# Optimization experiments

Measured on AMD Instinct MI355X. Metric: run time of the kernel, lower is better.

Reference implementation:

```python
import jax, jax.numpy as jnp
import numpy as np

N_NODES = 100000
N_EDGES = 1600000
N_GRAPHS = 256


def gcn_conv(x, src, dst, edge_weight, W, b, num_nodes):
    """PyG GCNConv: add self-loops, symmetric degree normalization,
    linear transform, scatter-add aggregation, bias."""
    loop = jnp.arange(num_nodes)
    s = jnp.concatenate([src, loop])
    d = jnp.concatenate([dst, loop])
    ew = jnp.concatenate([edge_weight, jnp.ones((num_nodes,), dtype=edge_weight.dtype)])
    deg = jax.ops.segment_sum(ew, d, num_segments=num_nodes)  # [N]
    dinv = jnp.where(deg > 0, deg ** -0.5, 0.0)
    norm = dinv[s] * ew * dinv[d]  # [E+N]
    h = x @ W  # [N, out]
    msg = h[s] * norm[:, None]  # gather + scale
    out = jax.ops.segment_sum(msg, d, num_segments=num_nodes)  # scatter-add
    return out + b


def global_mean_pool(x, batch, num_graphs):
    s = jax.ops.segment_sum(x, batch, num_segments=num_graphs)
    cnt = jax.ops.segment_sum(jnp.ones((x.shape[0],), dtype=x.dtype), batch, num_segments=num_graphs)
    return s / jnp.maximum(cnt, 1.0)[:, None]


def setup_inputs() -> dict:
    key = jax.random.key(0)
    ks = jax.random.split(key, 12)
    x = jax.random.normal(ks[0], (N_NODES, 128), dtype=jnp.float32)
    edge_index = jax.random.randint(ks[1], (2, N_EDGES), 0, N_NODES, dtype=jnp.int64)
    edge_attr = jax.random.uniform(ks[2], (N_EDGES,), dtype=jnp.float32)
    batch = jnp.sort(jax.random.randint(ks[3], (N_NODES,), 0, N_GRAPHS, dtype=jnp.int64))
    def lin(k, fan_in, fan_out):
        lim = 1.0 / np.sqrt(fan_in)
        kw, kb = jax.random.split(k)
        W = jax.random.uniform(kw, (fan_in, fan_out), minval=-lim, maxval=lim, dtype=jnp.float32)
        b = jax.random.uniform(kb, (fan_out,), minval=-lim, maxval=lim, dtype=jnp.float32)
        return W, b
    W1, b1 = lin(ks[4], 128, 64)
    W2, b2 = lin(ks[5], 64, 64)
    W3, b3 = lin(ks[6], 64, 64)
    Wl, bl = lin(ks[7], 64, 10)
    return {"x": x, "edge_index": edge_index, "edge_attr": edge_attr, "batch": batch,
            "W1": W1, "b1": b1, "W2": W2, "b2": b2, "W3": W3, "b3": b3, "Wl": Wl, "bl": bl}


def reference(x, edge_index, edge_attr, batch, W1, b1, W2, b2, W3, b3, Wl, bl):
    src, dst = edge_index[0], edge_index[1]
    n = x.shape[0]
    h = jax.nn.relu(gcn_conv(x, src, dst, edge_attr, W1, b1, n))
    h = jax.nn.relu(gcn_conv(h, src, dst, edge_attr, W2, b2, n))
    h = jax.nn.relu(gcn_conv(h, src, dst, edge_attr, W3, b3, n))
    g = global_mean_pool(h, batch, N_GRAPHS)  # [G, 64]
    return g @ Wl + bl  # [G, num_classes]
```

## Files before the change

### kernel.cpp

```cpp
#include <hip/hip_runtime.h>
#include <hip/hip_bf16.h>

#define N_NODES  100000
#define N_EDGES  1600000
#define N_GRAPHS 256
#define F 64
#define NBUCK  782
#define CHUNK  4096
#define NCHUNK 391


__global__ __launch_bounds__(1024) void k_hist(const int* __restrict__ dst, int* __restrict__ hist) {
    __shared__ int lh[NBUCK];
    int tid = threadIdx.x, chunk = blockIdx.x;
    for (int j = tid; j < NBUCK; j += 1024) lh[j] = 0;
    __syncthreads();
    int e0 = chunk * CHUNK;
#pragma unroll
    for (int i = 0; i < CHUNK / 1024; i++) {
        int e = e0 + i * 1024 + tid;
        if (e < N_EDGES) atomicAdd(&lh[dst[e] >> 7], 1);
    }
    __syncthreads();
    for (int j = tid; j < NBUCK; j += 1024) hist[chunk * NBUCK + j] = lh[j];
}

__global__ __launch_bounds__(512) void k_colscan(int* __restrict__ hist, int* __restrict__ btot) {
    __shared__ int ts[512];
    int b = blockIdx.x, tid = threadIdx.x;
    int v = (tid < NCHUNK) ? hist[tid * NBUCK + b] : 0;
    ts[tid] = v;
    __syncthreads();
    int x = v;
    for (int off = 1; off < 512; off <<= 1) {
        int t = (tid >= off) ? ts[tid - off] : 0;
        __syncthreads();
        x += t; ts[tid] = x;
        __syncthreads();
    }
    if (tid < NCHUNK) hist[tid * NBUCK + b] = x - v;
    if (tid == 511) btot[b] = x;
}

__global__ __launch_bounds__(256) void k_bscan(const int* __restrict__ btot, int* __restrict__ base) {
    __shared__ int ts[256];
    int tid = threadIdx.x;
    int v[4], loc[4], run = 0;
#pragma unroll
    for (int k = 0; k < 4; k++) {
        int c = tid * 4 + k;
        v[k] = (c < NBUCK) ? btot[c] : 0;
        loc[k] = run; run += v[k];
    }
    ts[tid] = run;
    __syncthreads();
    int x = run;
    for (int off = 1; off < 256; off <<= 1) {
        int t = (tid >= off) ? ts[tid - off] : 0;
        __syncthreads();
        x += t; ts[tid] = x;
        __syncthreads();
    }
    int texcl = x - run;
#pragma unroll
    for (int k = 0; k < 4; k++) {
        int c = tid * 4 + k;
        if (c < NBUCK) base[c] = texcl + loc[k];
    }
    if (tid == 255) base[NBUCK] = x;
}

__global__ __launch_bounds__(1024) void k_partition(const int* __restrict__ src, const int* __restrict__ dst,
                                                    const float* __restrict__ ew,
                                                    const int* __restrict__ hist, const int* __restrict__ base,
                                                    long long* __restrict__ part) {
    __shared__ int cursor[NBUCK];
    int tid = threadIdx.x, chunk = blockIdx.x;
    for (int j = tid; j < NBUCK; j += 1024) cursor[j] = base[j] + hist[chunk * NBUCK + j];
    __syncthreads();
    int e0 = chunk * CHUNK;
#pragma unroll
    for (int i = 0; i < CHUNK / 1024; i++) {
        int e = e0 + i * 1024 + tid;
        if (e < N_EDGES) {
            int d = dst[e];
            int pos = atomicAdd(&cursor[d >> 7], 1);
            unsigned lo = (unsigned)src[e] | ((unsigned)(d & 127) << 17);
            long long rec = (long long)((unsigned long long)lo |
                            ((unsigned long long)__float_as_uint(ew[e]) << 32));
            part[pos] = rec;
        }
    }
}

__global__ __launch_bounds__(256) void k_bucket(const long long* __restrict__ part,
                                                const int* __restrict__ base,
                                                float* __restrict__ dinv_g, int* __restrict__ row_off,
                                                int2* __restrict__ esec) {
    __shared__ float fdeg[128];
    __shared__ float sdinv[128];
    __shared__ int   cnt[128];
    __shared__ int   sc[128];
    __shared__ int   cursor[128];
    int b = blockIdx.x, tid = threadIdx.x;
    if (tid < 128) { fdeg[tid] = 1.0f; cnt[tid] = 0; }
    __syncthreads();
    int e0 = base[b], e1 = base[b + 1], ne = e1 - e0;
    for (int k = tid; k < ne; k += 256) {
        long long rec = part[e0 + k];
        int lo = (int)rec;
        int d7 = (lo >> 17) & 127;
        atomicAdd(&fdeg[d7], __uint_as_float((unsigned)(rec >> 32)));
        atomicAdd(&cnt[d7], 1);
    }
    __syncthreads();
    int myc = 0, x = 0;
    if (tid < 128) {
        float dv = rsqrtf(fdeg[tid]);
        sdinv[tid] = dv;
        int node = b * 128 + tid;
        if (node < N_NODES) dinv_g[node] = dv;
        myc = cnt[tid]; x = myc; sc[tid] = x;
    }
    __syncthreads();
    for (int off = 1; off < 128; off <<= 1) {
        int t = (tid < 128 && tid >= off) ? sc[tid - off] : 0;
        __syncthreads();
        if (tid < 128) { x += t; sc[tid] = x; }
        __syncthreads();
    }
    if (tid < 128) {
        int excl = x - myc;
        int node = b * 128 + tid;
        if (node < N_NODES) row_off[node] = e0 + excl;
        cursor[tid] = e0 + excl;
    }
    if (b == 0 && tid == 0) row_off[N_NODES] = N_EDGES;
    __syncthreads();
    for (int k = tid; k < ne; k += 256) {
        long long rec = part[e0 + k];
        int lo = (int)rec;
        int d7 = (lo >> 17) & 127;
        float w = __uint_as_float((unsigned)(rec >> 32));
        int pos = atomicAdd(&cursor[d7], 1);
        esec[pos] = make_int2((lo & 0x1FFFF) << 7, __float_as_int(w * sdinv[d7]));
    }
}

__global__ void k_coef(int2* __restrict__ esec, const float* __restrict__ dinv_g) {
    int e = blockIdx.x * 256 + threadIdx.x;
    if (e < N_EDGES) {
        int2 v = esec[e];
        esec[e] = make_int2(v.x, __float_as_int(__int_as_float(v.y) * dinv_g[((unsigned)v.x) >> 7]));
    } else if (e < N_EDGES + 16) {
        esec[e] = make_int2(0, 0);
    }
}

__global__ void k_gstart(const int* __restrict__ batch, int* gstart) {
    int g = blockIdx.x * 256 + threadIdx.x;
    if (g > N_GRAPHS) return;
    int lo = 0, hi = N_NODES;
    while (lo < hi) {
        int mid = (lo + hi) >> 1;
        if (batch[mid] < g) lo = mid + 1; else hi = mid;
    }
    gstart[g] = lo;
}

template <int K, bool BF16IN>
__global__ __launch_bounds__(256) void k_gemm(const void* __restrict__ Xv,
                                              const float* __restrict__ W,
                                              __hip_bfloat16* __restrict__ H) {
    constexpr int KC = 32;
    constexpr int XP = KC + 4;
    __shared__ float Xs[128 * XP];
    __shared__ float Ws[KC * F];
    const int tid  = threadIdx.x;
    const int fgrp = tid & 15;
    const int ngrp = tid >> 4;
    const int f0   = fgrp * 4;
    const int nb   = blockIdx.x * 128;

    float acc[8][4];
#pragma unroll
    for (int i = 0; i < 8; i++)
#pragma unroll
        for (int j = 0; j < 4; j++) acc[i][j] = 0.0f;

    for (int kc = 0; kc < K; kc += KC) {
        if (kc) __syncthreads();
        if (BF16IN) {
            const unsigned short* X = (const unsigned short*)Xv;
#pragma unroll
            for (int pass = 0; pass < 2; pass++) {
                int idx = tid + pass * 256;
                int r = idx >> 2, q = idx & 3;
                int gr = nb + r; if (gr >= N_NODES) gr = N_NODES - 1;
                uint4 v = *(const uint4*)&X[(size_t)gr * K + kc + q * 8];
                float* dp = &Xs[r * XP + q * 8];
                dp[0] = __uint_as_float(v.x << 16);
                dp[1] = __uint_as_float(v.x & 0xffff0000u);
                dp[2] = __uint_as_float(v.y << 16);
                dp[3] = __uint_as_float(v.y & 0xffff0000u);
                dp[4] = __uint_as_float(v.z << 16);
                dp[5] = __uint_as_float(v.z & 0xffff0000u);
                dp[6] = __uint_as_float(v.w << 16);
                dp[7] = __uint_as_float(v.w & 0xffff0000u);
            }
        } else {
            const float* X = (const float*)Xv;
#pragma unroll
            for (int pass = 0; pass < 4; pass++) {
                int idx = tid + pass * 256;
                int r = idx >> 3, q = idx & 7;
                int gr = nb + r; if (gr >= N_NODES) gr = N_NODES - 1;
                float4 v = *(const float4*)&X[(size_t)gr * K + kc + q * 4];
                *(float4*)&Xs[r * XP + q * 4] = v;
            }
        }
#pragma unroll
        for (int pass = 0; pass < 2; pass++) {
            int idx = tid + pass * 256;
            float4 v = *(const float4*)&W[(size_t)(kc + (idx >> 4)) * F + (idx & 15) * 4];
            *(float4*)&Ws[idx * 4] = v;
        }
        __syncthreads();
#pragma unroll
        for (int k = 0; k < KC; k += 4) {
            float4 wv[4];
#pragma unroll
            for (int kk = 0; kk < 4; kk++)
                wv[kk] = *(const float4*)&Ws[(k + kk) * F + f0];
#pragma unroll
            for (int i = 0; i < 8; i++) {
                float4 xv = *(const float4*)&Xs[(ngrp + 16 * i) * XP + k];
                acc[i][0] = fmaf(xv.x, wv[0].x, acc[i][0]);
                acc[i][0] = fmaf(xv.y, wv[1].x, acc[i][0]);
                acc[i][0] = fmaf(xv.z, wv[2].x, acc[i][0]);
                acc[i][0] = fmaf(xv.w, wv[3].x, acc[i][0]);
                acc[i][1] = fmaf(xv.x, wv[0].y, acc[i][1]);
                acc[i][1] = fmaf(xv.y, wv[1].y, acc[i][1]);
                acc[i][1] = fmaf(xv.z, wv[2].y, acc[i][1]);
                acc[i][1] = fmaf(xv.w, wv[3].y, acc[i][1]);
                acc[i][2] = fmaf(xv.x, wv[0].z, acc[i][2]);
                acc[i][2] = fmaf(xv.y, wv[1].z, acc[i][2]);
                acc[i][2] = fmaf(xv.z, wv[2].z, acc[i][2]);
                acc[i][2] = fmaf(xv.w, wv[3].z, acc[i][2]);
                acc[i][3] = fmaf(xv.x, wv[0].w, acc[i][3]);
                acc[i][3] = fmaf(xv.y, wv[1].w, acc[i][3]);
                acc[i][3] = fmaf(xv.z, wv[2].w, acc[i][3]);
                acc[i][3] = fmaf(xv.w, wv[3].w, acc[i][3]);
            }
        }
    }
#pragma unroll
    for (int i = 0; i < 8; i++) {
        int gn = nb + ngrp + 16 * i;
        if (gn < N_NODES) {
            __hip_bfloat16 hb[4];
            hb[0] = __float2bfloat16(acc[i][0]);
            hb[1] = __float2bfloat16(acc[i][1]);
            hb[2] = __float2bfloat16(acc[i][2]);
            hb[3] = __float2bfloat16(acc[i][3]);
            *(uint2*)&H[(size_t)gn * F + f0] = *(uint2*)hb;
        }
    }
}

__global__ __launch_bounds__(256) void k_agg(const __hip_bfloat16* __restrict__ H,
                                             const int* __restrict__ row_off,
                                             const int2* __restrict__ esec,
                                             const float* __restrict__ dinv,
                                             const float* __restrict__ bias,
                                             __hip_bfloat16* __restrict__ O) {
    int wv   = threadIdx.x >> 6;
    int lane = threadIdx.x & 63;
    int np   = blockIdx.x * 16 + wv * 4;
    int q  = lane >> 3;
    int f8 = lane & 7;
    int r0 = __builtin_amdgcn_readfirstlane(row_off[np]);
    int r1 = __builtin_amdgcn_readfirstlane(row_off[np + 1]);
    int r2 = __builtin_amdgcn_readfirstlane(row_off[np + 2]);
    int r3 = __builtin_amdgcn_readfirstlane(row_off[np + 3]);
    int r4 = __builtin_amdgcn_readfirstlane(row_off[np + 4]);
    const char* Hbase = (const char*)H;

    float a0[8], a1[8], a2[8], a3[8];
#pragma unroll
    for (int u = 0; u < 8; u++) { a0[u] = 0.0f; a1[u] = 0.0f; a2[u] = 0.0f; a3[u] = 0.0f; }

    int l0 = r1 - r0, l1 = r2 - r1, l2 = r3 - r2, l3 = r4 - r3;
    int ml = l0 > l1 ? l0 : l1;
    if (l2 > ml) ml = l2;
    if (l3 > ml) ml = l3;
    int iters = (ml + 7) >> 3;
    int j0 = r0 + q, j1 = r1 + q, j2 = r2 + q, j3 = r3 + q;
    for (int it = 0; it < iters; it++, j0 += 8, j1 += 8, j2 += 8, j3 += 8) {
        int i0 = j0 < N_EDGES ? j0 : N_EDGES;
        int i1 = j1 < N_EDGES ? j1 : N_EDGES;
        int i2 = j2 < N_EDGES ? j2 : N_EDGES;
        int i3 = j3 < N_EDGES ? j3 : N_EDGES;
        int2 ev0 = esec[i0];
        int2 ev1 = esec[i1];
        int2 ev2 = esec[i2];
        int2 ev3 = esec[i3];
        float c0 = (j0 < r1) ? __int_as_float(ev0.y) : 0.0f;
        float c1 = (j1 < r2) ? __int_as_float(ev1.y) : 0.0f;
        float c2 = (j2 < r3) ? __int_as_float(ev2.y) : 0.0f;
        float c3 = (j3 < r4) ? __int_as_float(ev3.y) : 0.0f;
        uint4 h0 = *(const uint4*)(Hbase + (unsigned)ev0.x + (f8 << 4));
        uint4 h1 = *(const uint4*)(Hbase + (unsigned)ev1.x + (f8 << 4));
        uint4 h2 = *(const uint4*)(Hbase + (unsigned)ev2.x + (f8 << 4));
        uint4 h3 = *(const uint4*)(Hbase + (unsigned)ev3.x + (f8 << 4));
        a0[0] = fmaf(c0, __uint_as_float(h0.x << 16),         a0[0]);
        a0[1] = fmaf(c0, __uint_as_float(h0.x & 0xffff0000u), a0[1]);
        a0[2] = fmaf(c0, __uint_as_float(h0.y << 16),         a0[2]);
        a0[3] = fmaf(c0, __uint_as_float(h0.y & 0xffff0000u), a0[3]);
        a0[4] = fmaf(c0, __uint_as_float(h0.z << 16),         a0[4]);
        a0[5] = fmaf(c0, __uint_as_float(h0.z & 0xffff0000u), a0[5]);
        a0[6] = fmaf(c0, __uint_as_float(h0.w << 16),         a0[6]);
        a0[7] = fmaf(c0, __uint_as_float(h0.w & 0xffff0000u), a0[7]);
        a1[0] = fmaf(c1, __uint_as_float(h1.x << 16),         a1[0]);
        a1[1] = fmaf(c1, __uint_as_float(h1.x & 0xffff0000u), a1[1]);
        a1[2] = fmaf(c1, __uint_as_float(h1.y << 16),         a1[2]);
        a1[3] = fmaf(c1, __uint_as_float(h1.y & 0xffff0000u), a1[3]);
        a1[4] = fmaf(c1, __uint_as_float(h1.z << 16),         a1[4]);
        a1[5] = fmaf(c1, __uint_as_float(h1.z & 0xffff0000u), a1[5]);
        a1[6] = fmaf(c1, __uint_as_float(h1.w << 16),         a1[6]);
        a1[7] = fmaf(c1, __uint_as_float(h1.w & 0xffff0000u), a1[7]);
        a2[0] = fmaf(c2, __uint_as_float(h2.x << 16),         a2[0]);
        a2[1] = fmaf(c2, __uint_as_float(h2.x & 0xffff0000u), a2[1]);
        a2[2] = fmaf(c2, __uint_as_float(h2.y << 16),         a2[2]);
        a2[3] = fmaf(c2, __uint_as_float(h2.y & 0xffff0000u), a2[3]);
        a2[4] = fmaf(c2, __uint_as_float(h2.z << 16),         a2[4]);
        a2[5] = fmaf(c2, __uint_as_float(h2.z & 0xffff0000u), a2[5]);
        a2[6] = fmaf(c2, __uint_as_float(h2.w << 16),         a2[6]);
        a2[7] = fmaf(c2, __uint_as_float(h2.w & 0xffff0000u), a2[7]);
        a3[0] = fmaf(c3, __uint_as_float(h3.x << 16),         a3[0]);
        a3[1] = fmaf(c3, __uint_as_float(h3.x & 0xffff0000u), a3[1]);
        a3[2] = fmaf(c3, __uint_as_float(h3.y << 16),         a3[2]);
        a3[3] = fmaf(c3, __uint_as_float(h3.y & 0xffff0000u), a3[3]);
        a3[4] = fmaf(c3, __uint_as_float(h3.z << 16),         a3[4]);
        a3[5] = fmaf(c3, __uint_as_float(h3.z & 0xffff0000u), a3[5]);
        a3[6] = fmaf(c3, __uint_as_float(h3.w << 16),         a3[6]);
        a3[7] = fmaf(c3, __uint_as_float(h3.w & 0xffff0000u), a3[7]);
    }
#pragma unroll
    for (int m = 8; m < 64; m <<= 1) {
#pragma unroll
        for (int u = 0; u < 8; u++) {
            a0[u] += __shfl_xor(a0[u], m);
            a1[u] += __shfl_xor(a1[u], m);
            a2[u] += __shfl_xor(a2[u], m);
            a3[u] += __shfl_xor(a3[u], m);
        }
    }
    if (q < 4) {
        int node = np + q;
        float av[8];
#pragma unroll
        for (int u = 0; u < 8; u++) {
            float t01 = (q & 1) ? a1[u] : a0[u];
            float t23 = (q & 1) ? a3[u] : a2[u];
            av[u] = (q & 2) ? t23 : t01;
        }
        float di = dinv[node];
        float di2 = di * di;
        uint4 hs = *(const uint4*)(Hbase + (size_t)node * 128 + (f8 << 4));
        float hv[8];
        hv[0] = __uint_as_float(hs.x << 16);
        hv[1] = __uint_as_float(hs.x & 0xffff0000u);
        hv[2] = __uint_as_float(hs.y << 16);
        hv[3] = __uint_as_float(hs.y & 0xffff0000u);
        hv[4] = __uint_as_float(hs.z << 16);
        hv[5] = __uint_as_float(hs.z & 0xffff0000u);
        hv[6] = __uint_as_float(hs.w << 16);
        hv[7] = __uint_as_float(hs.w & 0xffff0000u);
        const float4* bp = (const float4*)(bias + f8 * 8);
        float4 bv0 = bp[0], bv1 = bp[1];
        float r[8];
        r[0] = fmaxf(av[0] + bv0.x + di2 * hv[0], 0.0f);
        r[1] = fmaxf(av[1] + bv0.y + di2 * hv[1], 0.0f);
        r[2] = fmaxf(av[2] + bv0.z + di2 * hv[2], 0.0f);
        r[3] = fmaxf(av[3] + bv0.w + di2 * hv[3], 0.0f);
        r[4] = fmaxf(av[4] + bv1.x + di2 * hv[4], 0.0f);
        r[5] = fmaxf(av[5] + bv1.y + di2 * hv[5], 0.0f);
        r[6] = fmaxf(av[6] + bv1.z + di2 * hv[6], 0.0f);
        r[7] = fmaxf(av[7] + bv1.w + di2 * hv[7], 0.0f);
        __hip_bfloat16 hb[8];
#pragma unroll
        for (int u = 0; u < 8; u++) hb[u] = __float2bfloat16(r[u]);
        *(uint4*)&O[(size_t)node * F + f8 * 8] = *(uint4*)hb;
    }
}

__global__ __launch_bounds__(256) void k_pool_linear(const __hip_bfloat16* __restrict__ H,
                                                     const int* __restrict__ gstart,
                                                     const float* __restrict__ Wl,
                                                     const float* __restrict__ bl,
                                                     float* __restrict__ out) {
    int g = blockIdx.x;
    int beg = gstart[g], end = gstart[g + 1];
    int lane = threadIdx.x & 63, wv = threadIdx.x >> 6;
    float acc = 0.0f;
    for (int r = beg + wv; r < end; r += 4)
        acc += __bfloat162float(H[(size_t)r * F + lane]);
    __shared__ float s[4][F];
    s[wv][lane] = acc;
    __syncthreads();
    if (wv == 0) {
        float tot = s[0][lane] + s[1][lane] + s[2][lane] + s[3][lane];
        float cntf = (float)(end - beg);
        float p = tot / fmaxf(cntf, 1.0f);
        for (int c = 0; c < 10; c++) {
            float v = p * Wl[lane * 10 + c];
            for (int off = 32; off; off >>= 1) v += __shfl_down(v, off);
            if (lane == 0) out[g * 10 + c] = v + bl[c];
        }
    }
}


extern "C" void kernel_launch(void* const* d_in, const int* in_sizes, int n_in,
                              void* d_out, int out_size, void* d_ws, size_t ws_size,
                              hipStream_t stream) {
    const float* x    = (const float*)d_in[0];
    const int*   ei   = (const int*)d_in[1];
    const float* ea   = (const float*)d_in[2];
    const int*   bat  = (const int*)d_in[3];
    const float* W1   = (const float*)d_in[4];
    const float* b1   = (const float*)d_in[5];
    const float* W2   = (const float*)d_in[6];
    const float* b2   = (const float*)d_in[7];
    const float* W3   = (const float*)d_in[8];
    const float* b3   = (const float*)d_in[9];
    const float* Wl   = (const float*)d_in[10];
    const float* bl   = (const float*)d_in[11];
    float* out = (float*)d_out;

    const int* src = ei;
    const int* dst = ei + N_EDGES;

    char* ws = (char*)d_ws;
    size_t off = 0;
    auto carve = [&](size_t bytes) {
        void* p = ws + off;
        off += (bytes + 255) & ~(size_t)255;
        return p;
    };
    float*          dinv    = (float*)carve(N_NODES * 4);
    int*            row_off = (int*)  carve((N_NODES + 1) * 4);
    int2*           esec    = (int2*) carve(((size_t)N_EDGES + 16) * 8);
    __hip_bfloat16* hbuf    = (__hip_bfloat16*)carve((size_t)N_NODES * F * 2);
    __hip_bfloat16* obuf    = (__hip_bfloat16*)carve((size_t)N_NODES * F * 4);
    int*            gstart  = (int*)  carve((N_GRAPHS + 1) * 4);
    (void)ws_size; (void)in_sizes; (void)n_in; (void)out_size;

    long long* part = (long long*)hbuf;
    char* alias = (char*)obuf + (size_t)N_NODES * F * 2;
    int* hist = (int*)alias;                         alias += (size_t)NCHUNK * NBUCK * 4;
    int* btot = (int*)alias;                         alias += (NBUCK + 8) * 4;
    int* base = (int*)alias;

    const int EB  = (N_EDGES + 255) / 256 + 1;
    const int GB  = (N_NODES + 127) / 128;

    k_hist     <<<NCHUNK, 1024, 0, stream>>>(dst, hist);
    k_colscan  <<<NBUCK,  512,  0, stream>>>(hist, btot);
    k_bscan    <<<1,      256,  0, stream>>>(btot, base);
    k_partition<<<NCHUNK, 1024, 0, stream>>>(src, dst, ea, hist, base, part);
    k_bucket   <<<NBUCK,  256,  0, stream>>>(part, base, dinv, row_off, esec);
    k_coef     <<<EB,     256,  0, stream>>>(esec, dinv);
    k_gstart   <<<2,      256,  0, stream>>>(bat, gstart);

    k_gemm<128, false><<<GB, 256, 0, stream>>>(x, W1, hbuf);
    k_agg<<<N_NODES / 16, 256, 0, stream>>>(hbuf, row_off, esec, dinv, b1, obuf);
    k_gemm<64, true><<<GB, 256, 0, stream>>>(obuf, W2, hbuf);
    k_agg<<<N_NODES / 16, 256, 0, stream>>>(hbuf, row_off, esec, dinv, b2, obuf);
    k_gemm<64, true><<<GB, 256, 0, stream>>>(obuf, W3, hbuf);
    k_agg<<<N_NODES / 16, 256, 0, stream>>>(hbuf, row_off, esec, dinv, b3, obuf);

    k_pool_linear<<<N_GRAPHS, 256, 0, stream>>>(obuf, gstart, Wl, bl, out);
}
```

Baseline: 380.4 us.

## Split bucket kernel into degree and scatter passes, fuse coef and gstart, widen GEMM tile

The old k_bucket plus k_coef pair becomes k_deg and k_scat. k_scat computes the full normalization coefficient inline, which removes a separate pass over the 1.6M-entry edge array. The gstart binary search is merged into the bucket-scan launch as a second block, which saves one launch. The feature-transform GEMM moves to 256-node tiles with 8 outputs per thread, doubling shared memory and accumulator registers in exchange for more reuse of each weight load. k_scat reads dinv_g[s] as a random global gather and reads the partitioned records a second time.

```diff
diff --git a/kernel.cpp b/kernel.cpp
--- a/kernel.cpp
+++ b/kernel.cpp
@@ -42,32 +42,48 @@
     if (tid == 511) btot[b] = x;
 }
 
-__global__ __launch_bounds__(256) void k_bscan(const int* __restrict__ btot, int* __restrict__ base) {
+__global__ __launch_bounds__(512) void k_bscan_gstart(const int* __restrict__ btot, int* __restrict__ base,
+                                                      const int* __restrict__ batch, int* __restrict__ gstart) {
+    if (blockIdx.x == 1) {
+        int g = threadIdx.x;
+        if (g > N_GRAPHS) return;
+        int lo = 0, hi = N_NODES;
+        while (lo < hi) {
+            int mid = (lo + hi) >> 1;
+            if (batch[mid] < g) lo = mid + 1; else hi = mid;
+        }
+        gstart[g] = lo;
+        return;
+    }
     __shared__ int ts[256];
     int tid = threadIdx.x;
     int v[4], loc[4], run = 0;
-#pragma unroll
-    for (int k = 0; k < 4; k++) {
-        int c = tid * 4 + k;
-        v[k] = (c < NBUCK) ? btot[c] : 0;
-        loc[k] = run; run += v[k];
-    }
-    ts[tid] = run;
+    if (tid < 256) {
+#pragma unroll
+        for (int k = 0; k < 4; k++) {
+            int c = tid * 4 + k;
+            v[k] = (c < NBUCK) ? btot[c] : 0;
+            loc[k] = run; run += v[k];
+        }
+        ts[tid] = run;
+    }
     __syncthreads();
     int x = run;
     for (int off = 1; off < 256; off <<= 1) {
-        int t = (tid >= off) ? ts[tid - off] : 0;
-        __syncthreads();
-        x += t; ts[tid] = x;
-        __syncthreads();
-    }
-    int texcl = x - run;
-#pragma unroll
-    for (int k = 0; k < 4; k++) {
-        int c = tid * 4 + k;
-        if (c < NBUCK) base[c] = texcl + loc[k];
-    }
-    if (tid == 255) base[NBUCK] = x;
+        int t = (tid >= off && tid < 256) ? ts[tid - off] : 0;
+        __syncthreads();
+        if (tid < 256) { x += t; ts[tid] = x; }
+        __syncthreads();
+    }
+    if (tid < 256) {
+        int texcl = x - run;
+#pragma unroll
+        for (int k = 0; k < 4; k++) {
+            int c = tid * 4 + k;
+            if (c < NBUCK) base[c] = texcl + loc[k];
+        }
+        if (tid == 255) base[NBUCK] = x;
+    }
 }
 
 __global__ __launch_bounds__(1024) void k_partition(const int* __restrict__ src, const int* __restrict__ dst,
@@ -93,79 +109,69 @@
     }
 }
 
-__global__ __launch_bounds__(256) void k_bucket(const long long* __restrict__ part,
-                                                const int* __restrict__ base,
-                                                float* __restrict__ dinv_g, int* __restrict__ row_off,
-                                                int2* __restrict__ esec) {
+__global__ __launch_bounds__(512) void k_deg(const long long* __restrict__ part,
+                                             const int* __restrict__ base,
+                                             float* __restrict__ dinv_g, int* __restrict__ row_off) {
     __shared__ float fdeg[128];
-    __shared__ float sdinv[128];
     __shared__ int   cnt[128];
     __shared__ int   sc[128];
-    __shared__ int   cursor[128];
     int b = blockIdx.x, tid = threadIdx.x;
     if (tid < 128) { fdeg[tid] = 1.0f; cnt[tid] = 0; }
     __syncthreads();
-    int e0 = base[b], e1 = base[b + 1], ne = e1 - e0;
-    for (int k = tid; k < ne; k += 256) {
-        long long rec = part[e0 + k];
+    int e0 = base[b], e1 = base[b + 1];
+    for (int k = e0 + tid; k < e1; k += 512) {
+        long long rec = part[k];
+        int d7 = ((int)rec >> 17) & 127;
+        atomicAdd(&fdeg[d7], __uint_as_float((unsigned)(rec >> 32)));
+        atomicAdd(&cnt[d7], 1);
+    }
+    __syncthreads();
+    int myc = 0, x = 0;
+    if (tid < 128) {
+        int node = b * 128 + tid;
+        if (node < N_NODES) dinv_g[node] = rsqrtf(fdeg[tid]);
+        myc = cnt[tid]; x = myc; sc[tid] = x;
+    }
+    __syncthreads();
+    for (int off = 1; off < 128; off <<= 1) {
+        int t = (tid < 128 && tid >= off) ? sc[tid - off] : 0;
+        __syncthreads();
+        if (tid < 128) { x += t; sc[tid] = x; }
+        __syncthreads();
+    }
+    if (tid < 128) {
+        int node = b * 128 + tid;
+        if (node < N_NODES) row_off[node] = e0 + (x - myc);
+    }
+    if (b == 0 && tid == 0) row_off[N_NODES] = N_EDGES;
+}
+
+__global__ __launch_bounds__(512) void k_scat(const long long* __restrict__ part,
+                                              const int* __restrict__ base,
+                                              const float* __restrict__ dinv_g,
+                                              const int* __restrict__ row_off,
+                                              int2* __restrict__ esec) {
+    __shared__ int   cursor[128];
+    __shared__ float sdinv[128];
+    int b = blockIdx.x, tid = threadIdx.x;
+    if (tid < 128) {
+        int node = b * 128 + tid;
+        cursor[tid] = row_off[node < N_NODES ? node : N_NODES];
+        sdinv[tid]  = dinv_g[node < N_NODES ? node : 0];
+    }
+    __syncthreads();
+    int e0 = base[b], e1 = base[b + 1];
+    for (int k = e0 + tid; k < e1; k += 512) {
+        long long rec = part[k];
         int lo = (int)rec;
         int d7 = (lo >> 17) & 127;
-        atomicAdd(&fdeg[d7], __uint_as_float((unsigned)(rec >> 32)));
-        atomicAdd(&cnt[d7], 1);
-    }
-    __syncthreads();
-    int myc = 0, x = 0;
-    if (tid < 128) {
-        float dv = rsqrtf(fdeg[tid]);
-        sdinv[tid] = dv;
-        int node = b * 128 + tid;
-        if (node < N_NODES) dinv_g[node] = dv;
-        myc = cnt[tid]; x = myc; sc[tid] = x;
-    }
-    __syncthreads();
-    for (int off = 1; off < 128; off <<= 1) {
-        int t = (tid < 128 && tid >= off) ? sc[tid - off] : 0;
-        __syncthreads();
-        if (tid < 128) { x += t; sc[tid] = x; }
-        __syncthreads();
-    }
-    if (tid < 128) {
-        int excl = x - myc;
-        int node = b * 128 + tid;
-        if (node < N_NODES) row_off[node] = e0 + excl;
-        cursor[tid] = e0 + excl;
-    }
-    if (b == 0 && tid == 0) row_off[N_NODES] = N_EDGES;
-    __syncthreads();
-    for (int k = tid; k < ne; k += 256) {
-        long long rec = part[e0 + k];
-        int lo = (int)rec;
-        int d7 = (lo >> 17) & 127;
+        int s  = lo & 0x1FFFF;
         float w = __uint_as_float((unsigned)(rec >> 32));
+        float coef = (w * sdinv[d7]) * dinv_g[s];
         int pos = atomicAdd(&cursor[d7], 1);
-        esec[pos] = make_int2((lo & 0x1FFFF) << 7, __float_as_int(w * sdinv[d7]));
-    }
-}
-
-__global__ void k_coef(int2* __restrict__ esec, const float* __restrict__ dinv_g) {
-    int e = blockIdx.x * 256 + threadIdx.x;
-    if (e < N_EDGES) {
-        int2 v = esec[e];
-        esec[e] = make_int2(v.x, __float_as_int(__int_as_float(v.y) * dinv_g[((unsigned)v.x) >> 7]));
-    } else if (e < N_EDGES + 16) {
-        esec[e] = make_int2(0, 0);
-    }
-}
-
-__global__ void k_gstart(const int* __restrict__ batch, int* gstart) {
-    int g = blockIdx.x * 256 + threadIdx.x;
-    if (g > N_GRAPHS) return;
-    int lo = 0, hi = N_NODES;
-    while (lo < hi) {
-        int mid = (lo + hi) >> 1;
-        if (batch[mid] < g) lo = mid + 1; else hi = mid;
-    }
-    gstart[g] = lo;
+        esec[pos] = make_int2(s << 7, __float_as_int(coef));
+    }
+    if (b == 0 && tid < 16) esec[N_EDGES + tid] = make_int2(0, 0);
 }
 
 template <int K, bool BF16IN>
@@ -174,26 +180,26 @@
                                               __hip_bfloat16* __restrict__ H) {
     constexpr int KC = 32;
     constexpr int XP = KC + 4;
-    __shared__ float Xs[128 * XP];
+    __shared__ float Xs[256 * XP];
     __shared__ float Ws[KC * F];
     const int tid  = threadIdx.x;
-    const int fgrp = tid & 15;
-    const int ngrp = tid >> 4;
-    const int f0   = fgrp * 4;
-    const int nb   = blockIdx.x * 128;
-
-    float acc[8][4];
+    const int fgrp = tid & 7;
+    const int ngrp = tid >> 3;
+    const int f0   = fgrp * 8;
+    const int nb   = blockIdx.x * 256;
+
+    float acc[8][8];
 #pragma unroll
     for (int i = 0; i < 8; i++)
 #pragma unroll
-        for (int j = 0; j < 4; j++) acc[i][j] = 0.0f;
+        for (int j = 0; j < 8; j++) acc[i][j] = 0.0f;
 
     for (int kc = 0; kc < K; kc += KC) {
         if (kc) __syncthreads();
         if (BF16IN) {
             const unsigned short* X = (const unsigned short*)Xv;
 #pragma unroll
-            for (int pass = 0; pass < 2; pass++) {
+            for (int pass = 0; pass < 4; pass++) {
                 int idx = tid + pass * 256;
                 int r = idx >> 2, q = idx & 3;
                 int gr = nb + r; if (gr >= N_NODES) gr = N_NODES - 1;
@@ -211,7 +217,7 @@
         } else {
             const float* X = (const float*)Xv;
 #pragma unroll
-            for (int pass = 0; pass < 4; pass++) {
+            for (int pass = 0; pass < 8; pass++) {
                 int idx = tid + pass * 256;
                 int r = idx >> 3, q = idx & 7;
                 int gr = nb + r; if (gr >= N_NODES) gr = N_NODES - 1;
@@ -228,42 +234,38 @@
         __syncthreads();
 #pragma unroll
         for (int k = 0; k < KC; k += 4) {
-            float4 wv[4];
-#pragma unroll
-            for (int kk = 0; kk < 4; kk++)
-                wv[kk] = *(const float4*)&Ws[(k + kk) * F + f0];
+            float4 wa[4], wb[4];
+#pragma unroll
+            for (int kk = 0; kk < 4; kk++) {
+                wa[kk] = *(const float4*)&Ws[(k + kk) * F + f0];
+                wb[kk] = *(const float4*)&Ws[(k + kk) * F + f0 + 4];
+            }
 #pragma unroll
             for (int i = 0; i < 8; i++) {
-                float4 xv = *(const float4*)&Xs[(ngrp + 16 * i) * XP + k];
-                acc[i][0] = fmaf(xv.x, wv[0].x, acc[i][0]);
-                acc[i][0] = fmaf(xv.y, wv[1].x, acc[i][0]);
-                acc[i][0] = fmaf(xv.z, wv[2].x, acc[i][0]);
-                acc[i][0] = fmaf(xv.w, wv[3].x, acc[i][0]);
-                acc[i][1] = fmaf(xv.x, wv[0].y, acc[i][1]);
-                acc[i][1] = fmaf(xv.y, wv[1].y, acc[i][1]);
-                acc[i][1] = fmaf(xv.z, wv[2].y, acc[i][1]);
-                acc[i][1] = fmaf(xv.w, wv[3].y, acc[i][1]);
-                acc[i][2] = fmaf(xv.x, wv[0].z, acc[i][2]);
-                acc[i][2] = fmaf(xv.y, wv[1].z, acc[i][2]);
-                acc[i][2] = fmaf(xv.z, wv[2].z, acc[i][2]);
-                acc[i][2] = fmaf(xv.w, wv[3].z, acc[i][2]);
-                acc[i][3] = fmaf(xv.x, wv[0].w, acc[i][3]);
-                acc[i][3] = fmaf(xv.y, wv[1].w, acc[i][3]);
-                acc[i][3] = fmaf(xv.z, wv[2].w, acc[i][3]);
-                acc[i][3] = fmaf(xv.w, wv[3].w, acc[i][3]);
+                float4 xv = *(const float4*)&Xs[(ngrp + 32 * i) * XP + k];
+#pragma unroll
+                for (int kk = 0; kk < 4; kk++) {
+                    float xk = (kk == 0) ? xv.x : (kk == 1) ? xv.y : (kk == 2) ? xv.z : xv.w;
+                    acc[i][0] = fmaf(xk, wa[kk].x, acc[i][0]);
+                    acc[i][1] = fmaf(xk, wa[kk].y, acc[i][1]);
+                    acc[i][2] = fmaf(xk, wa[kk].z, acc[i][2]);
+                    acc[i][3] = fmaf(xk, wa[kk].w, acc[i][3]);
+                    acc[i][4] = fmaf(xk, wb[kk].x, acc[i][4]);
+                    acc[i][5] = fmaf(xk, wb[kk].y, acc[i][5]);
+                    acc[i][6] = fmaf(xk, wb[kk].z, acc[i][6]);
+                    acc[i][7] = fmaf(xk, wb[kk].w, acc[i][7]);
+                }
             }
         }
     }
 #pragma unroll
     for (int i = 0; i < 8; i++) {
-        int gn = nb + ngrp + 16 * i;
+        int gn = nb + ngrp + 32 * i;
         if (gn < N_NODES) {
-            __hip_bfloat16 hb[4];
-            hb[0] = __float2bfloat16(acc[i][0]);
-            hb[1] = __float2bfloat16(acc[i][1]);
-            hb[2] = __float2bfloat16(acc[i][2]);
-            hb[3] = __float2bfloat16(acc[i][3]);
-            *(uint2*)&H[(size_t)gn * F + f0] = *(uint2*)hb;
+            __hip_bfloat16 hb[8];
+#pragma unroll
+            for (int j = 0; j < 8; j++) hb[j] = __float2bfloat16(acc[i][j]);
+            *(uint4*)&H[(size_t)gn * F + f0] = *(uint4*)hb;
         }
     }
 }
@@ -463,16 +465,14 @@
     int* btot = (int*)alias;                         alias += (NBUCK + 8) * 4;
     int* base = (int*)alias;
 
-    const int EB  = (N_EDGES + 255) / 256 + 1;
-    const int GB  = (N_NODES + 127) / 128;
-
-    k_hist     <<<NCHUNK, 1024, 0, stream>>>(dst, hist);
-    k_colscan  <<<NBUCK,  512,  0, stream>>>(hist, btot);
-    k_bscan    <<<1,      256,  0, stream>>>(btot, base);
-    k_partition<<<NCHUNK, 1024, 0, stream>>>(src, dst, ea, hist, base, part);
-    k_bucket   <<<NBUCK,  256,  0, stream>>>(part, base, dinv, row_off, esec);
-    k_coef     <<<EB,     256,  0, stream>>>(esec, dinv);
-    k_gstart   <<<2,      256,  0, stream>>>(bat, gstart);
+    const int GB = (N_NODES + 255) / 256;
+
+    k_hist        <<<NCHUNK, 1024, 0, stream>>>(dst, hist);
+    k_colscan     <<<NBUCK,  512,  0, stream>>>(hist, btot);
+    k_bscan_gstart<<<2,      512,  0, stream>>>(btot, base, bat, gstart);
+    k_partition   <<<NCHUNK, 1024, 0, stream>>>(src, dst, ea, hist, base, part);
+    k_deg         <<<NBUCK,  512,  0, stream>>>(part, base, dinv, row_off);
+    k_scat        <<<NBUCK,  512,  0, stream>>>(part, base, dinv, row_off, esec);
 
     k_gemm<128, false><<<GB, 256, 0, stream>>>(x, W1, hbuf);
     k_agg<<<N_NODES / 16, 256, 0, stream>>>(hbuf, row_off, esec, dinv, b1, obuf);
```

New measurement: 382.1 us. No clear change (+0.5%).
